# Kernel tuning notes

Measured on AMD Instinct MI355X. Metric: run time of the kernel, lower is better.

## Reference

```python
import jax, jax.numpy as jnp
import numpy as np

B, A, N, P, D, H = 2, 9, 1024, 4, 256, 8
DH = D // H
EPS = 1e-12


def _layernorm(x, gamma, beta):
    m = jnp.mean(x, axis=-1, keepdims=True)
    v = jnp.var(x, axis=-1, keepdims=True)
    return (x - m) / jnp.sqrt(v + EPS) * gamma + beta


def setup_inputs() -> dict:
    key = jax.random.key(0)
    ks = jax.random.split(key, 10)
    # adjacency stacks A relation matrices; scale 1/N keeps the P-step matmul chain O(1)
    adjacency = jax.random.uniform(ks[0], (B, A, N, N), jnp.float32) / N
    # diagonal, strictly positive degree matrix -> invertible
    diag = 1.0 + jax.random.uniform(ks[1], (B, N), jnp.float32)
    degree = jax.vmap(jnp.diag)(diag)
    x = jax.random.normal(ks[2], (B, N, D), jnp.float32)
    # per-head params stacked on leading H axis
    kernels = 0.1 * jax.random.normal(ks[3], (H, A, P), jnp.float32)  # RandomNormal(0, 0.1)
    lim = np.sqrt(6.0 / D).astype(np.float32)
    Wv = jax.random.uniform(ks[4], (H, D, DH), jnp.float32, -lim, lim)  # he_uniform
    Bv = jnp.zeros((H, N, DH), jnp.float32)
    W0 = jax.random.uniform(ks[5], (D, D), jnp.float32, -lim, lim)
    gamma2 = jnp.ones((D,), jnp.float32)
    beta2 = jnp.zeros((D,), jnp.float32)
    W1 = jax.random.normal(ks[6], (D, 2 * D), jnp.float32) * np.sqrt(2.0 / D).astype(np.float32)
    b1 = jnp.zeros((2 * D,), jnp.float32)
    gf = jnp.ones((2 * D,), jnp.float32)
    bf = jnp.zeros((2 * D,), jnp.float32)
    W2 = jax.random.normal(ks[7], (2 * D, D), jnp.float32) * np.sqrt(2.0 / (2 * D)).astype(np.float32)
    b2f = jnp.zeros((D,), jnp.float32)
    return {"adjacency": adjacency, "degree": degree, "x": x, "kernels": kernels,
            "Wv": Wv, "Bv": Bv, "W0": W0, "gamma2": gamma2, "beta2": beta2,
            "W1": W1, "b1": b1, "gf": gf, "bf": bf, "W2": W2, "b2f": b2f}


def reference(adjacency, degree, x, kernels, Wv, Bv, W0, gamma2, beta2, W1, b1, gf, bf, W2, b2f):
    # ---- AdjacencyAggregator (all H heads batched on leading axis) ----
    # softmax(relu(kernel)) over the input-channel (relation) axis
    soft = jax.nn.softmax(jax.nn.relu(kernels), axis=-2)  # [H, A, P]
    # 1x1 conv == per-position convex mix of the A relation matrices, one mix per path step
    # sequential chain: meta = M_0 @ M_1 @ ... @ M_{P-1}   (P is small and fixed)
    result = jnp.einsum('banm,ha->hbnm', adjacency, soft[:, :, 0])  # [H, B, N, N]
    for i in range(1, P):
        mi = jnp.einsum('banm,ha->hbnm', adjacency, soft[:, :, i])
        result = jnp.matmul(result, mi)
    inv_deg = jnp.linalg.inv(degree)                # [B, N, N], shared across heads
    normed = jnp.matmul(inv_deg[None], result)      # [H, B, N, N]
    # ---- MetaPathHead value projection + message passing ----
    V = jnp.einsum('bnd,hde->hbne', x, Wv) + Bv[:, None]   # [H, B, N, DH]
    heads = jnp.matmul(normed, V)                          # [H, B, N, DH]
    # concat along feature axis in head order
    attn = jnp.transpose(heads, (1, 2, 0, 3)).reshape(B, N, D)
    # ---- outer block: W0, residual, pre-norm FFN ----
    residual = attn @ W0 + x
    h = _layernorm(residual, gamma2, beta2)
    f = jax.nn.gelu(h @ W1 + b1, approximate=False)
    f = _layernorm(f, gf, bf)
    out = f @ W2 + b2f + residual
    return out
```

## Files before the change

### kernel.cpp

```cpp
#include <hip/hip_runtime.h>
#include <hip/hip_bf16.h>
#include <math.h>

#define B_ 2
#define A_ 9
#define N_ 1024
#define P_ 4
#define D_ 256
#define H_ 8
#define DH_ 32
#define ROWS_ (B_*N_)
#define KS_ 8
#define ADJ_ELEMS_ ((size_t)B_*A_*N_*N_)
#define SLABF4_ 131072

typedef __attribute__((ext_vector_type(8))) short bf16x8;
typedef __attribute__((ext_vector_type(4))) float f32x4;

__device__ __forceinline__ uint pack2_bf(float x, float y) {
    uint ux = __float_as_uint(x); ux += 0x7fffu + ((ux >> 16) & 1u);
    uint uy = __float_as_uint(y); uy += 0x7fffu + ((uy >> 16) & 1u);
    return (ux >> 16) | (uy & 0xffff0000u);
}
__device__ __forceinline__ float bflo(uint u){ return __uint_as_float(u << 16); }
__device__ __forceinline__ float bfhi(uint u){ return __uint_as_float(u & 0xffff0000u); }

__global__ void prep_kernel(const float* __restrict__ kernels, const float* __restrict__ degree,
                            float* __restrict__ soft, float* __restrict__ invd)
{
    int t = threadIdx.x;
    if (blockIdx.x == 0) {
        if (t < H_*P_) {
            int h = t >> 2, p = t & 3;
            float vals[A_];
            float m = 0.0f;
            #pragma unroll
            for (int a = 0; a < A_; a++) {
                float v = kernels[h*A_*P_ + a*P_ + p];
                v = v > 0.0f ? v : 0.0f;
                vals[a] = v;
                m = fmaxf(m, v);
            }
            float s = 0.0f;
            #pragma unroll
            for (int a = 0; a < A_; a++) { vals[a] = expf(vals[a] - m); s += vals[a]; }
            float inv = 1.0f / s;
            #pragma unroll
            for (int a = 0; a < A_; a++) soft[h*A_*P_ + a*P_ + p] = vals[a] * inv;
        }
    } else {
        int idx = (blockIdx.x - 1) * 256 + t;
        if (idx < ROWS_) {
            int b = idx >> 10, n = idx & (N_-1);
            invd[idx] = 1.0f / degree[(size_t)b*N_*N_ + (size_t)n*N_ + n];
        }
    }
}

__global__ void adj_pack_kernel(const float* __restrict__ in, ushort* __restrict__ out)
{
    int j = blockIdx.x * 256 + threadIdx.x;
    int kk8   = j & 3;
    int r     = (j >> 2) & 15;
    int t     = j >> 6;
    int a     = t % 9;
    int rest  = t / 9;
    int chunk = rest & 3;
    int ks    = (rest >> 2) & 7;
    int rowblk= (rest >> 5) & 63;
    int b     = rest >> 11;
    const float* src = &in[(((size_t)b*A_ + a)*N_ + (rowblk*16 + r))*N_ + ks*128 + chunk*32 + kk8*8];
    float4 v0 = *(const float4*)src;
    float4 v1 = *(const float4*)(src + 4);
    uint4 o;
    o.x = pack2_bf(v0.x, v0.y);
    o.y = pack2_bf(v0.z, v0.w);
    o.z = pack2_bf(v1.x, v1.y);
    o.w = pack2_bf(v1.z, v1.w);
    ((uint4*)out)[j] = o;
}

__global__ __launch_bounds__(256, 4)
void chain_mfma(const ushort* __restrict__ adjp, const float* __restrict__ soft,
                const ushort* __restrict__ Tin, float* __restrict__ Pp, int step)
{
    __shared__ __align__(16) ushort smem[8*640 + 16*648];
    __shared__ float soft_s[8][9];
    ushort* sm_ms = smem;
    ushort* sm_t  = smem + 8*640;

    int bid    = blockIdx.x;
    int ks     = bid & (KS_-1);
    int rowblk = (bid >> 3) & 63;
    int b      = bid >> 9;
    int n0     = rowblk * 16;
    int tid    = threadIdx.x;
    int lane   = tid & 63;
    int w      = tid >> 6;

    if (tid < 72) { int h = tid/9, a = tid%9; soft_s[h][a] = soft[h*A_*P_ + a*P_ + step]; }
    __syncthreads();

    int mr   = tid >> 4;
    int mk2  = (tid & 15) * 2;
    int mk2s = mk2 ^ ((mr & 3) << 3);
    const ushort* ablk = adjp + (size_t)((b*64 + rowblk)*8 + ks) * 18432;

    int sp  = tid >> 4;
    int sk0 = (tid & 15) * 2;
    const ushort* tbase = Tin + ((size_t)(b*16 + sp)*1024 + (size_t)ks*128) * 16;

    int g   = lane >> 4;
    int c15 = lane & 15;
    int gx  = (g ^ (c15 & 3)) * 8;

    f32x4 acc[4];
    #pragma unroll
    for (int j = 0; j < 4; j++) acc[j] = (f32x4){0.f, 0.f, 0.f, 0.f};

    for (int chunk = 0; chunk < 4; chunk++) {
        uint av[9];
        {
            const ushort* asl = ablk + chunk*4608 + mk2;
            #pragma unroll
            for (int a = 0; a < A_; a++) av[a] = *(const uint*)&asl[(a*16 + mr)*32];
        }
        const ushort* tsl = tbase + (size_t)(chunk*32 + sk0) * 16;
        uint4 q0 = *(const uint4*)(tsl + 0);
        uint4 q1 = *(const uint4*)(tsl + 8);
        uint4 q2 = *(const uint4*)(tsl + 16);
        uint4 q3 = *(const uint4*)(tsl + 24);

        if (chunk) __syncthreads();

        {
            float va0[9], va1[9];
            #pragma unroll
            for (int a = 0; a < A_; a++) { va0[a] = bflo(av[a]); va1[a] = bfhi(av[a]); }
            #pragma unroll
            for (int h = 0; h < H_; h++) {
                float s0 = soft_s[h][0]*va0[0];
                float s1 = soft_s[h][0]*va1[0];
                #pragma unroll
                for (int a = 1; a < A_; a++) { s0 += soft_s[h][a]*va0[a]; s1 += soft_s[h][a]*va1[a]; }
                *(uint*)&sm_ms[h*640 + mr*40 + mk2s] = pack2_bf(s0, s1);
            }
        }
        {
            uint l0[4] = {q0.x, q0.y, q0.z, q0.w};
            uint l1[4] = {q1.x, q1.y, q1.z, q1.w};
            uint h0[4] = {q2.x, q2.y, q2.z, q2.w};
            uint h1[4] = {q3.x, q3.y, q3.z, q3.w};
            #pragma unroll
            for (int ci = 0; ci < 8; ci++) {
                uint a0 = (l0[ci>>1] >> ((ci&1)*16)) & 0xffffu;
                uint b0 = (h0[ci>>1] >> ((ci&1)*16)) & 0xffffu;
                int k0s = sk0 ^ ((ci & 3) << 3);
                *(uint*)&sm_t[sp*648 + ci*40 + k0s] = a0 | (b0 << 16);
            }
            #pragma unroll
            for (int ci = 0; ci < 8; ci++) {
                int c = ci + 8;
                uint a0 = (l1[ci>>1] >> ((ci&1)*16)) & 0xffffu;
                uint b0 = (h1[ci>>1] >> ((ci&1)*16)) & 0xffffu;
                int k0s = sk0 ^ ((c & 3) << 3);
                *(uint*)&sm_t[sp*648 + c*40 + k0s] = a0 | (b0 << 16);
            }
        }
        __syncthreads();

        {
            const ushort* mb = sm_ms + c15*40 + gx;
            const ushort* tb = sm_t  + c15*40 + gx;
            #pragma unroll
            for (int j = 0; j < 4; j++) {
                int cg = w + 4*j;
                int h  = cg >> 1;
                bf16x8 af  = *(const bf16x8*)&mb[h*640];
                bf16x8 bfr = *(const bf16x8*)&tb[cg*648];
                acc[j] = __builtin_amdgcn_mfma_f32_16x16x32_bf16(af, bfr, acc[j], 0, 0, 0);
            }
        }
    }

    __syncthreads();
    float* Ep = (float*)smem;
    #pragma unroll
    for (int j = 0; j < 4; j++) {
        int cg = w + 4*j;
        #pragma unroll
        for (int i = 0; i < 4; i++)
            Ep[cg*256 + (g*4 + i)*16 + c15] = acc[j][i];
    }
    __syncthreads();
    {
        int p = tid >> 4, r = tid & 15;
        float* dst = Pp + (((size_t)(ks*B_ + b)*16 + p)*N_ + (n0 + r)) * 16;
        const float* src = &Ep[p*256 + r*16];
        *(float4*)&dst[0]  = *(const float4*)&src[0];
        *(float4*)&dst[4]  = *(const float4*)&src[4];
        *(float4*)&dst[8]  = *(const float4*)&src[8];
        *(float4*)&dst[12] = *(const float4*)&src[12];
    }
}

template<int FINAL>
__global__ void chain_reduce(const float* __restrict__ Pp, ushort* __restrict__ outp,
                             const float* __restrict__ invd)
{
    int pidx = blockIdx.x * 256 + threadIdx.x;
    float4 s = make_float4(0.f, 0.f, 0.f, 0.f);
    #pragma unroll
    for (int ks = 0; ks < KS_; ks++) {
        float4 v = ((const float4*)Pp)[(size_t)ks*SLABF4_ + pidx];
        s.x += v.x; s.y += v.y; s.z += v.z; s.w += v.w;
    }
    if constexpr (FINAL) {
        int lin = pidx * 4;
        int n  = (lin >> 4) & (N_-1);
        int b  = lin >> 18;
        float sc = invd[b*N_ + n];
        s.x *= sc; s.y *= sc; s.z *= sc; s.w *= sc;
    }
    uint2 wv;
    wv.x = pack2_bf(s.x, s.y);
    wv.y = pack2_bf(s.z, s.w);
    ((uint2*)outp)[pidx] = wv;
}

#define BK 16
__global__ void gemm_v(const float* __restrict__ A, const float* __restrict__ Bm,
                       const float* __restrict__ bias, ushort* __restrict__ C)
{
    __shared__ __align__(16) float As[BK][68];
    __shared__ __align__(16) float Bs[BK][68];
    int m0 = blockIdx.x * 64;
    int n0 = blockIdx.y * 64;
    int tid = threadIdx.x;
    int tx = tid & 15, ty = tid >> 4;

    float acc[4][4];
    #pragma unroll
    for (int i = 0; i < 4; i++)
        #pragma unroll
        for (int j = 0; j < 4; j++) acc[i][j] = 0.0f;

    for (int k0 = 0; k0 < D_; k0 += BK) {
        {
            int m = tid >> 2;
            int k = (tid & 3) * 4;
            float4 v = *(const float4*)&A[(size_t)(m0+m)*D_ + k0 + k];
            As[k+0][m] = v.x; As[k+1][m] = v.y; As[k+2][m] = v.z; As[k+3][m] = v.w;
        }
        {
            int k = tid >> 4;
            int n = (tid & 15) * 4;
            int c = n0 + n; int h = c >> 5; int ee = c & 31;
            float4 v = *(const float4*)&Bm[(size_t)h*D_*DH_ + (size_t)(k0+k)*DH_ + ee];
            *(float4*)&Bs[k][n] = v;
        }
        __syncthreads();
        #pragma unroll
        for (int k = 0; k < BK; k++) {
            float4 a4 = *(const float4*)&As[k][ty*4];
            float4 b4 = *(const float4*)&Bs[k][tx*4];
            acc[0][0] += a4.x*b4.x; acc[0][1] += a4.x*b4.y; acc[0][2] += a4.x*b4.z; acc[0][3] += a4.x*b4.w;
            acc[1][0] += a4.y*b4.x; acc[1][1] += a4.y*b4.y; acc[1][2] += a4.y*b4.z; acc[1][3] += a4.y*b4.w;
            acc[2][0] += a4.z*b4.x; acc[2][1] += a4.z*b4.y; acc[2][2] += a4.z*b4.z; acc[2][3] += a4.z*b4.w;
            acc[3][0] += a4.w*b4.x; acc[3][1] += a4.w*b4.y; acc[3][2] += a4.w*b4.z; acc[3][3] += a4.w*b4.w;
        }
        __syncthreads();
    }

    #pragma unroll
    for (int i = 0; i < 4; i++) {
        int row  = m0 + ty*4 + i;
        int nloc = n0 + tx*4;
        float o[4];
        #pragma unroll
        for (int j = 0; j < 4; j++) {
            int c = nloc + j;
            int h = c >> 5, ee = c & 31, n = row & (N_-1);
            o[j] = acc[i][j] + bias[(size_t)h*N_*DH_ + (size_t)n*DH_ + ee];
        }
        int bb = row >> 10, n = row & (N_-1);
        int cg = nloc >> 4, cc = nloc & 15;
        uint2 wv;
        wv.x = pack2_bf(o[0], o[1]);
        wv.y = pack2_bf(o[2], o[3]);
        *(uint2*)&C[(((size_t)bb*16 + cg)*N_ + n)*16 + cc] = wv;
    }
}


__global__ __launch_bounds__(256, 2)
void gemm_r(const ushort* __restrict__ attnp, const float* __restrict__ W0,
            const float* __restrict__ x, const float* __restrict__ gamma,
            const float* __restrict__ beta, float* __restrict__ resid,
            ushort* __restrict__ hbuf)
{
    __shared__ __align__(16) ushort As[16*40];
    __shared__ __align__(16) ushort Bs[256*40];
    __shared__ float lnb[16*257];
    __shared__ float2 stat[16];

    int m0 = blockIdx.x * 16;
    int b16 = (m0 >> 10) * 16;
    int nb  = m0 & (N_-1);
    int tid = threadIdx.x;
    int lane = tid & 63;
    int w = tid >> 6;
    int g = lane >> 4, c15 = lane & 15;
    int gx = (g ^ (c15 & 3)) * 8;

    int am = tid >> 4, ak2 = (tid & 15) * 2;
    int apos = am*40 + ((((ak2>>3) ^ (am&3))) << 3) + (ak2 & 7);
    int bn8 = (tid & 31) * 8;
    int bkq = (tid >> 5) * 4;
    int bpos0 = (((bkq>>3)) << 3) + (bkq & 7);

    f32x4 acc[4];
    #pragma unroll
    for (int j = 0; j < 4; j++) acc[j] = (f32x4){0.f,0.f,0.f,0.f};

    for (int ks = 0; ks < 8; ks++) {
        int k0 = ks * 32;
        int k = k0 + ak2;
        uint av = *(const uint*)&attnp[(((size_t)(b16 + (k>>4)))*N_ + nb + am)*16 + (k & 15)];
        float4 lo[4], hi[4];
        #pragma unroll
        for (int i = 0; i < 4; i++) {
            lo[i] = *(const float4*)&W0[(size_t)(k0+bkq+i)*D_ + bn8];
            hi[i] = *(const float4*)&W0[(size_t)(k0+bkq+i)*D_ + bn8 + 4];
        }
        if (ks) __syncthreads();
        *(uint*)&As[apos] = av;
        #pragma unroll
        for (int jn = 0; jn < 8; jn++) {
            int n = bn8 + jn;
            float v0 = (jn<4)? ((const float*)&lo[0])[jn] : ((const float*)&hi[0])[jn-4];
            float v1 = (jn<4)? ((const float*)&lo[1])[jn] : ((const float*)&hi[1])[jn-4];
            float v2 = (jn<4)? ((const float*)&lo[2])[jn] : ((const float*)&hi[2])[jn-4];
            float v3 = (jn<4)? ((const float*)&lo[3])[jn] : ((const float*)&hi[3])[jn-4];
            uint2 wv; wv.x = pack2_bf(v0, v1); wv.y = pack2_bf(v2, v3);
            *(uint2*)&Bs[n*40 + (bpos0 ^ ((n&3)<<3))] = wv;
        }
        __syncthreads();
        const ushort* ab = As + c15*40 + gx;
        #pragma unroll
        for (int nt = 0; nt < 4; nt++) {
            int n = w*64 + nt*16 + c15;
            bf16x8 af  = *(const bf16x8*)ab;
            bf16x8 bfr = *(const bf16x8*)&Bs[n*40 + gx];
            acc[nt] = __builtin_amdgcn_mfma_f32_16x16x32_bf16(af, bfr, acc[nt], 0, 0, 0);
        }
    }
    __syncthreads();

    #pragma unroll
    for (int nt = 0; nt < 4; nt++) {
        int c = w*64 + nt*16 + c15;
        #pragma unroll
        for (int i = 0; i < 4; i++) {
            int r = g*4 + i;
            lnb[r*257 + c] = acc[nt][i] + x[(size_t)(m0+r)*D_ + c];
        }
    }
    __syncthreads();

    {
        int rr = tid >> 4, sl = tid & 15;
        float sum = 0.f, sq = 0.f;
        #pragma unroll
        for (int j = 0; j < 16; j++) {
            float v = lnb[rr*257 + sl + 16*j];
            sum += v; sq += v*v;
        }
        #pragma unroll
        for (int m = 1; m < 16; m <<= 1) { sum += __shfl_xor(sum, m); sq += __shfl_xor(sq, m); }
        if (sl == 0) {
            float mean = sum * (1.0f/D_);
            float var  = fmaxf(sq * (1.0f/D_) - mean*mean, 0.f);
            stat[rr] = make_float2(mean, rsqrtf(var + 1e-12f));
        }
    }
    __syncthreads();

    {
        int rr = tid & 15, s2 = tid >> 4;
        float2 ms = stat[rr];
        int c0 = s2 * 16;
        uint hw[8];
        #pragma unroll
        for (int q = 0; q < 4; q++) {
            int c = c0 + q*4;
            float4 v = *(const float4*)&lnb[rr*257 + c];
            *(float4*)&resid[(size_t)(m0+rr)*D_ + c] = v;
            float4 gm = *(const float4*)&gamma[c];
            float4 bt = *(const float4*)&beta[c];
            float h0 = (v.x - ms.x)*ms.y*gm.x + bt.x;
            float h1 = (v.y - ms.x)*ms.y*gm.y + bt.y;
            float h2 = (v.z - ms.x)*ms.y*gm.z + bt.z;
            float h3 = (v.w - ms.x)*ms.y*gm.w + bt.w;
            hw[2*q]   = pack2_bf(h0, h1);
            hw[2*q+1] = pack2_bf(h2, h3);
        }
        ushort* hp = &hbuf[(size_t)(m0+rr)*D_ + c0];
        *(uint4*)&hp[0] = make_uint4(hw[0], hw[1], hw[2], hw[3]);
        *(uint4*)&hp[8] = make_uint4(hw[4], hw[5], hw[6], hw[7]);
    }
}

__global__ __launch_bounds__(256, 2)
void gemm_f1(const ushort* __restrict__ hbuf, const float* __restrict__ W1,
             const float* __restrict__ b1, const float* __restrict__ gf,
             const float* __restrict__ bfv, ushort* __restrict__ fout)
{
    __shared__ __align__(16) ushort As[16*40];
    __shared__ __align__(16) ushort Bs[512*40];
    __shared__ float lnb[16*513];
    __shared__ float2 stat[16];

    int m0 = blockIdx.x * 16;
    int tid = threadIdx.x;
    int lane = tid & 63;
    int w = tid >> 6;
    int g = lane >> 4, c15 = lane & 15;
    int gx = (g ^ (c15 & 3)) * 8;

    int am = tid >> 4, ak2 = (tid & 15) * 2;
    int apos = am*40 + ((((ak2>>3) ^ (am&3))) << 3) + (ak2 & 7);
    int bn8 = (tid & 63) * 8;
    int bk8 = (tid >> 6) * 8;

    f32x4 acc[8];
    #pragma unroll
    for (int j = 0; j < 8; j++) acc[j] = (f32x4){0.f,0.f,0.f,0.f};

    for (int ks = 0; ks < 8; ks++) {
        int k0 = ks * 32;
        uint av = *(const uint*)&hbuf[(size_t)(m0+am)*D_ + k0 + ak2];
        float4 q[16];
        #pragma unroll
        for (int i = 0; i < 8; i++) {
            q[2*i]   = *(const float4*)&W1[(size_t)(k0+bk8+i)*(2*D_) + bn8];
            q[2*i+1] = *(const float4*)&W1[(size_t)(k0+bk8+i)*(2*D_) + bn8 + 4];
        }
        if (ks) __syncthreads();
        *(uint*)&As[apos] = av;
        #pragma unroll
        for (int jn = 0; jn < 8; jn++) {
            int n = bn8 + jn;
            float e0 = (jn<4)? ((const float*)&q[0])[jn]  : ((const float*)&q[1])[jn-4];
            float e1 = (jn<4)? ((const float*)&q[2])[jn]  : ((const float*)&q[3])[jn-4];
            float e2 = (jn<4)? ((const float*)&q[4])[jn]  : ((const float*)&q[5])[jn-4];
            float e3 = (jn<4)? ((const float*)&q[6])[jn]  : ((const float*)&q[7])[jn-4];
            float e4 = (jn<4)? ((const float*)&q[8])[jn]  : ((const float*)&q[9])[jn-4];
            float e5 = (jn<4)? ((const float*)&q[10])[jn] : ((const float*)&q[11])[jn-4];
            float e6 = (jn<4)? ((const float*)&q[12])[jn] : ((const float*)&q[13])[jn-4];
            float e7 = (jn<4)? ((const float*)&q[14])[jn] : ((const float*)&q[15])[jn-4];
            uint4 wv;
            wv.x = pack2_bf(e0, e1); wv.y = pack2_bf(e2, e3);
            wv.z = pack2_bf(e4, e5); wv.w = pack2_bf(e6, e7);
            *(uint4*)&Bs[n*40 + ((((bk8>>3) ^ (n&3))) << 3)] = wv;
        }
        __syncthreads();
        const ushort* ab = As + c15*40 + gx;
        #pragma unroll
        for (int nt = 0; nt < 8; nt++) {
            int n = w*128 + nt*16 + c15;
            bf16x8 af  = *(const bf16x8*)ab;
            bf16x8 bfr = *(const bf16x8*)&Bs[n*40 + gx];
            acc[nt] = __builtin_amdgcn_mfma_f32_16x16x32_bf16(af, bfr, acc[nt], 0, 0, 0);
        }
    }
    __syncthreads();

    #pragma unroll
    for (int nt = 0; nt < 8; nt++) {
        int c = w*128 + nt*16 + c15;
        float bias = b1[c];
        #pragma unroll
        for (int i = 0; i < 4; i++) {
            int r = g*4 + i;
            float v = acc[nt][i] + bias;
            v = 0.5f * v * (1.0f + erff(v * 0.70710678118654752f));
            lnb[r*513 + c] = v;
        }
    }
    __syncthreads();

    {
        int rr = tid >> 4, sl = tid & 15;
        float sum = 0.f, sq = 0.f;
        #pragma unroll
        for (int j = 0; j < 32; j++) {
            float v = lnb[rr*513 + sl + 16*j];
            sum += v; sq += v*v;
        }
        #pragma unroll
        for (int m = 1; m < 16; m <<= 1) { sum += __shfl_xor(sum, m); sq += __shfl_xor(sq, m); }
        if (sl == 0) {
            float mean = sum * (1.0f/(2*D_));
            float var  = fmaxf(sq * (1.0f/(2*D_)) - mean*mean, 0.f);
            stat[rr] = make_float2(mean, rsqrtf(var + 1e-12f));
        }
    }
    __syncthreads();

    {
        int rr = tid & 15, s2 = tid >> 4;
        float2 ms = stat[rr];
        int c0 = s2 * 32;
        #pragma unroll
        for (int q = 0; q < 8; q++) {
            int c = c0 + q*4;
            float4 v = *(const float4*)&lnb[rr*513 + c];
            float4 gm = *(const float4*)&gf[c];
            float4 bt = *(const float4*)&bfv[c];
            float h0 = (v.x - ms.x)*ms.y*gm.x + bt.x;
            float h1 = (v.y - ms.x)*ms.y*gm.y + bt.y;
            float h2 = (v.z - ms.x)*ms.y*gm.z + bt.z;
            float h3 = (v.w - ms.x)*ms.y*gm.w + bt.w;
            *(uint2*)&fout[(size_t)(m0+rr)*(2*D_) + c] = make_uint2(pack2_bf(h0,h1), pack2_bf(h2,h3));
        }
    }
}

__global__ __launch_bounds__(256, 2)
void gemm_f2(const ushort* __restrict__ fbuf, const float* __restrict__ W2,
             const float* __restrict__ b2f, const float* __restrict__ resid,
             float* __restrict__ outp)
{
    __shared__ __align__(16) ushort As[16*40];
    __shared__ __align__(16) ushort Bs[256*40];
    __shared__ float lnb[16*257];

    int m0 = blockIdx.x * 16;
    int tid = threadIdx.x;
    int lane = tid & 63;
    int w = tid >> 6;
    int g = lane >> 4, c15 = lane & 15;
    int gx = (g ^ (c15 & 3)) * 8;

    int am = tid >> 4, ak2 = (tid & 15) * 2;
    int apos = am*40 + ((((ak2>>3) ^ (am&3))) << 3) + (ak2 & 7);
    int bn8 = (tid & 31) * 8;
    int bkq = (tid >> 5) * 4;
    int bpos0 = (((bkq>>3)) << 3) + (bkq & 7);

    f32x4 acc[4];
    #pragma unroll
    for (int j = 0; j < 4; j++) acc[j] = (f32x4){0.f,0.f,0.f,0.f};

    for (int ks = 0; ks < 16; ks++) {
        int k0 = ks * 32;
        uint av = *(const uint*)&fbuf[(size_t)(m0+am)*(2*D_) + k0 + ak2];
        float4 lo[4], hi[4];
        #pragma unroll
        for (int i = 0; i < 4; i++) {
            lo[i] = *(const float4*)&W2[(size_t)(k0+bkq+i)*D_ + bn8];
            hi[i] = *(const float4*)&W2[(size_t)(k0+bkq+i)*D_ + bn8 + 4];
        }
        if (ks) __syncthreads();
        *(uint*)&As[apos] = av;
        #pragma unroll
        for (int jn = 0; jn < 8; jn++) {
            int n = bn8 + jn;
            float v0 = (jn<4)? ((const float*)&lo[0])[jn] : ((const float*)&hi[0])[jn-4];
            float v1 = (jn<4)? ((const float*)&lo[1])[jn] : ((const float*)&hi[1])[jn-4];
            float v2 = (jn<4)? ((const float*)&lo[2])[jn] : ((const float*)&hi[2])[jn-4];
            float v3 = (jn<4)? ((const float*)&lo[3])[jn] : ((const float*)&hi[3])[jn-4];
            uint2 wv; wv.x = pack2_bf(v0, v1); wv.y = pack2_bf(v2, v3);
            *(uint2*)&Bs[n*40 + (bpos0 ^ ((n&3)<<3))] = wv;
        }
        __syncthreads();
        const ushort* ab = As + c15*40 + gx;
        #pragma unroll
        for (int nt = 0; nt < 4; nt++) {
            int n = w*64 + nt*16 + c15;
            bf16x8 af  = *(const bf16x8*)ab;
            bf16x8 bfr = *(const bf16x8*)&Bs[n*40 + gx];
            acc[nt] = __builtin_amdgcn_mfma_f32_16x16x32_bf16(af, bfr, acc[nt], 0, 0, 0);
        }
    }
    __syncthreads();

    #pragma unroll
    for (int nt = 0; nt < 4; nt++) {
        int c = w*64 + nt*16 + c15;
        #pragma unroll
        for (int i = 0; i < 4; i++)
            lnb[(g*4+i)*257 + c] = acc[nt][i];
    }
    __syncthreads();

    {
        int rr = tid & 15, s2 = tid >> 4;
        int c0 = s2 * 16;
        #pragma unroll
        for (int q = 0; q < 4; q++) {
            int c = c0 + q*4;
            float4 v  = *(const float4*)&lnb[rr*257 + c];
            float4 bb = *(const float4*)&b2f[c];
            float4 rs = *(const float4*)&resid[(size_t)(m0+rr)*D_ + c];
            float4 o = make_float4(v.x+bb.x+rs.x, v.y+bb.y+rs.y, v.z+bb.z+rs.z, v.w+bb.w+rs.w);
            *(float4*)&outp[(size_t)(m0+rr)*D_ + c] = o;
        }
    }
}

extern "C" void kernel_launch(void* const* d_in, const int* in_sizes, int n_in,
                              void* d_out, int out_size, void* d_ws, size_t ws_size,
                              hipStream_t stream)
{
    const float* adj    = (const float*)d_in[0];
    const float* degree = (const float*)d_in[1];
    const float* x      = (const float*)d_in[2];
    const float* kern   = (const float*)d_in[3];
    const float* Wv     = (const float*)d_in[4];
    const float* Bv     = (const float*)d_in[5];
    const float* W0     = (const float*)d_in[6];
    const float* gamma2 = (const float*)d_in[7];
    const float* beta2  = (const float*)d_in[8];
    const float* W1     = (const float*)d_in[9];
    const float* b1     = (const float*)d_in[10];
    const float* gf     = (const float*)d_in[11];
    const float* bf_    = (const float*)d_in[12];
    const float* W2     = (const float*)d_in[13];
    const float* b2f    = (const float*)d_in[14];
    float* out = (float*)d_out;
    float* ws  = (float*)d_ws;

    size_t off = 0;
    float* soft  = ws + off; off += 512;
    float* invd  = ws + off; off += 2048;
    float* T0    = ws + off; off += (size_t)ROWS_*D_;
    float* T1    = ws + off; off += (size_t)ROWS_*D_;
    float* resid = ws + off; off += (size_t)ROWS_*D_;
    float* hbuf  = ws + off; off += (size_t)ROWS_*D_;
    float* fbuf  = ws + off; off += (size_t)ROWS_*2*D_;
    float* fbuf2 = ws + off; off += (size_t)ROWS_*2*D_;
    float* Pp    = ws + off; off += (size_t)KS_*ROWS_*D_;
    ushort* adjp = (ushort*)(ws + off);
    (void)fbuf2;

    ushort* T0b = (ushort*)T0;
    ushort* T1b = (ushort*)T1;
    ushort* hb  = (ushort*)hbuf;
    ushort* fb  = (ushort*)fbuf;

    prep_kernel<<<9, 256, 0, stream>>>(kern, degree, soft, invd);
    adj_pack_kernel<<<(int)(ADJ_ELEMS_/8/256), 256, 0, stream>>>(adj, adjp);
    gemm_v<<<dim3(ROWS_/64, D_/64), 256, 0, stream>>>(x, Wv, Bv, T0b);

    int chain_grid  = B_*64*KS_;
    int reduce_grid = SLABF4_/256;
    chain_mfma<<<chain_grid, 256, 0, stream>>>(adjp, soft, T0b, Pp, 3);
    chain_reduce<0><<<reduce_grid, 256, 0, stream>>>(Pp, T1b, invd);
    chain_mfma<<<chain_grid, 256, 0, stream>>>(adjp, soft, T1b, Pp, 2);
    chain_reduce<0><<<reduce_grid, 256, 0, stream>>>(Pp, T0b, invd);
    chain_mfma<<<chain_grid, 256, 0, stream>>>(adjp, soft, T0b, Pp, 1);
    chain_reduce<0><<<reduce_grid, 256, 0, stream>>>(Pp, T1b, invd);
    chain_mfma<<<chain_grid, 256, 0, stream>>>(adjp, soft, T1b, Pp, 0);
    chain_reduce<1><<<reduce_grid, 256, 0, stream>>>(Pp, T0b, invd);

    gemm_r <<<ROWS_/16, 256, 0, stream>>>(T0b, W0, x, gamma2, beta2, resid, hb);
    gemm_f1<<<ROWS_/16, 256, 0, stream>>>(hb, W1, b1, gf, bf_, fb);
    gemm_f2<<<ROWS_/16, 256, 0, stream>>>(fb, W2, b2f, resid, out);
}
```

Before: 200.5 us.

## Fuse adjacency bf16 packing into first chain step and final reduce into W0 GEMM

Removes the separate adjacency pack kernel: the first chain_mfma step reads fp32 adjacency directly, uses it, and writes the packed bf16 copy that later steps read. The last split-K reduce and the inverse-degree scaling move into gemm_r, which sums the eight partial slabs while loading its A tile. The three tail GEMMs switch from 16 to 8 rows per block with higher occupancy bounds, so they launch twice as many blocks, but half the threads sit idle in the A load and epilogue phases.

```diff
diff --git a/kernel.cpp b/kernel.cpp
--- a/kernel.cpp
+++ b/kernel.cpp
@@ -12,7 +12,8 @@
 #define ROWS_ (B_*N_)
 #define KS_ 8
 #define ADJ_ELEMS_ ((size_t)B_*A_*N_*N_)
-#define SLABF4_ 131072
+#define SLABF_ 524288
+#define SLABF4_ (SLABF_/4)
 
 typedef __attribute__((ext_vector_type(8))) short bf16x8;
 typedef __attribute__((ext_vector_type(4))) float f32x4;
@@ -57,31 +58,10 @@
     }
 }
 
-__global__ void adj_pack_kernel(const float* __restrict__ in, ushort* __restrict__ out)
-{
-    int j = blockIdx.x * 256 + threadIdx.x;
-    int kk8   = j & 3;
-    int r     = (j >> 2) & 15;
-    int t     = j >> 6;
-    int a     = t % 9;
-    int rest  = t / 9;
-    int chunk = rest & 3;
-    int ks    = (rest >> 2) & 7;
-    int rowblk= (rest >> 5) & 63;
-    int b     = rest >> 11;
-    const float* src = &in[(((size_t)b*A_ + a)*N_ + (rowblk*16 + r))*N_ + ks*128 + chunk*32 + kk8*8];
-    float4 v0 = *(const float4*)src;
-    float4 v1 = *(const float4*)(src + 4);
-    uint4 o;
-    o.x = pack2_bf(v0.x, v0.y);
-    o.y = pack2_bf(v0.z, v0.w);
-    o.z = pack2_bf(v1.x, v1.y);
-    o.w = pack2_bf(v1.z, v1.w);
-    ((uint4*)out)[j] = o;
-}
-
+template<int PACK>
 __global__ __launch_bounds__(256, 4)
-void chain_mfma(const ushort* __restrict__ adjp, const float* __restrict__ soft,
+void chain_mfma(const float* __restrict__ adjf, ushort* __restrict__ adjp,
+                const float* __restrict__ soft,
                 const ushort* __restrict__ Tin, float* __restrict__ Pp, int step)
 {
     __shared__ __align__(16) ushort smem[8*640 + 16*648];
@@ -104,7 +84,7 @@
     int mr   = tid >> 4;
     int mk2  = (tid & 15) * 2;
     int mk2s = mk2 ^ ((mr & 3) << 3);
-    const ushort* ablk = adjp + (size_t)((b*64 + rowblk)*8 + ks) * 18432;
+    ushort* ablk = adjp + (size_t)((b*64 + rowblk)*8 + ks) * 18432;
 
     int sp  = tid >> 4;
     int sk0 = (tid & 15) * 2;
@@ -119,11 +99,20 @@
     for (int j = 0; j < 4; j++) acc[j] = (f32x4){0.f, 0.f, 0.f, 0.f};
 
     for (int chunk = 0; chunk < 4; chunk++) {
-        uint av[9];
-        {
-            const ushort* asl = ablk + chunk*4608 + mk2;
-            #pragma unroll
-            for (int a = 0; a < A_; a++) av[a] = *(const uint*)&asl[(a*16 + mr)*32];
+        float lo[9], hi[9];
+        if constexpr (PACK) {
+            #pragma unroll
+            for (int a = 0; a < A_; a++) {
+                float2 v = *(const float2*)&adjf[(((size_t)b*A_ + a)*N_ + (n0+mr))*N_
+                                                 + ks*128 + chunk*32 + mk2];
+                lo[a] = v.x; hi[a] = v.y;
+            }
+        } else {
+            #pragma unroll
+            for (int a = 0; a < A_; a++) {
+                uint av = *(const uint*)&ablk[chunk*4608 + (a*16 + mr)*32 + mk2];
+                lo[a] = bflo(av); hi[a] = bfhi(av);
+            }
         }
         const ushort* tsl = tbase + (size_t)(chunk*32 + sk0) * 16;
         uint4 q0 = *(const uint4*)(tsl + 0);
@@ -131,20 +120,21 @@
         uint4 q2 = *(const uint4*)(tsl + 16);
         uint4 q3 = *(const uint4*)(tsl + 24);
 
+        if constexpr (PACK) {
+            #pragma unroll
+            for (int a = 0; a < A_; a++)
+                *(uint*)&ablk[chunk*4608 + (a*16 + mr)*32 + mk2] = pack2_bf(lo[a], hi[a]);
+        }
+
         if (chunk) __syncthreads();
 
-        {
-            float va0[9], va1[9];
-            #pragma unroll
-            for (int a = 0; a < A_; a++) { va0[a] = bflo(av[a]); va1[a] = bfhi(av[a]); }
-            #pragma unroll
-            for (int h = 0; h < H_; h++) {
-                float s0 = soft_s[h][0]*va0[0];
-                float s1 = soft_s[h][0]*va1[0];
-                #pragma unroll
-                for (int a = 1; a < A_; a++) { s0 += soft_s[h][a]*va0[a]; s1 += soft_s[h][a]*va1[a]; }
-                *(uint*)&sm_ms[h*640 + mr*40 + mk2s] = pack2_bf(s0, s1);
-            }
+        #pragma unroll
+        for (int h = 0; h < H_; h++) {
+            float s0 = soft_s[h][0]*lo[0];
+            float s1 = soft_s[h][0]*hi[0];
+            #pragma unroll
+            for (int a = 1; a < A_; a++) { s0 += soft_s[h][a]*lo[a]; s1 += soft_s[h][a]*hi[a]; }
+            *(uint*)&sm_ms[h*640 + mr*40 + mk2s] = pack2_bf(s0, s1);
         }
         {
             uint l0[4] = {q0.x, q0.y, q0.z, q0.w};
@@ -204,9 +194,7 @@
     }
 }
 
-template<int FINAL>
-__global__ void chain_reduce(const float* __restrict__ Pp, ushort* __restrict__ outp,
-                             const float* __restrict__ invd)
+__global__ void chain_reduce(const float* __restrict__ Pp, ushort* __restrict__ outp)
 {
     int pidx = blockIdx.x * 256 + threadIdx.x;
     float4 s = make_float4(0.f, 0.f, 0.f, 0.f);
@@ -214,13 +202,6 @@
     for (int ks = 0; ks < KS_; ks++) {
         float4 v = ((const float4*)Pp)[(size_t)ks*SLABF4_ + pidx];
         s.x += v.x; s.y += v.y; s.z += v.z; s.w += v.w;
-    }
-    if constexpr (FINAL) {
-        int lin = pidx * 4;
-        int n  = (lin >> 4) & (N_-1);
-        int b  = lin >> 18;
-        float sc = invd[b*N_ + n];
-        s.x *= sc; s.y *= sc; s.z *= sc; s.w *= sc;
     }
     uint2 wv;
     wv.x = pack2_bf(s.x, s.y);
@@ -293,48 +274,61 @@
 }
 
 
-__global__ __launch_bounds__(256, 2)
-void gemm_r(const ushort* __restrict__ attnp, const float* __restrict__ W0,
-            const float* __restrict__ x, const float* __restrict__ gamma,
-            const float* __restrict__ beta, float* __restrict__ resid,
-            ushort* __restrict__ hbuf)
+__global__ __launch_bounds__(256, 4)
+void gemm_r(const float* __restrict__ Pp, const float* __restrict__ invd,
+            const float* __restrict__ W0, const float* __restrict__ x,
+            const float* __restrict__ gamma, const float* __restrict__ beta,
+            float* __restrict__ resid, ushort* __restrict__ hbuf)
 {
     __shared__ __align__(16) ushort As[16*40];
     __shared__ __align__(16) ushort Bs[256*40];
-    __shared__ float lnb[16*257];
-    __shared__ float2 stat[16];
-
-    int m0 = blockIdx.x * 16;
-    int b16 = (m0 >> 10) * 16;
-    int nb  = m0 & (N_-1);
+    __shared__ float lnb[8*257];
+    __shared__ float2 stat[8];
+
+    int m0 = blockIdx.x * 8;
+    int b  = m0 >> 10;
+    int nb = m0 & (N_-1);
     int tid = threadIdx.x;
     int lane = tid & 63;
     int w = tid >> 6;
     int g = lane >> 4, c15 = lane & 15;
     int gx = (g ^ (c15 & 3)) * 8;
 
-    int am = tid >> 4, ak2 = (tid & 15) * 2;
+    int am  = tid >> 4;
+    int ak2 = (tid & 15) * 2;
     int apos = am*40 + ((((ak2>>3) ^ (am&3))) << 3) + (ak2 & 7);
+    float idv = (tid < 128) ? invd[b*N_ + nb + am] : 0.f;
+
     int bn8 = (tid & 31) * 8;
     int bkq = (tid >> 5) * 4;
-    int bpos0 = (((bkq>>3)) << 3) + (bkq & 7);
+    int bposR = ((bkq >> 3) << 3) + (bkq & 7);
 
     f32x4 acc[4];
     #pragma unroll
     for (int j = 0; j < 4; j++) acc[j] = (f32x4){0.f,0.f,0.f,0.f};
 
-    for (int ks = 0; ks < 8; ks++) {
-        int k0 = ks * 32;
-        int k = k0 + ak2;
-        uint av = *(const uint*)&attnp[(((size_t)(b16 + (k>>4)))*N_ + nb + am)*16 + (k & 15)];
+    for (int ksi = 0; ksi < 8; ksi++) {
+        int k0 = ksi * 32;
+        uint av = 0;
+        if (tid < 128) {
+            int k = k0 + ak2;
+            size_t base = (((size_t)(b*16 + (k>>4)))*N_ + nb + am)*16 + (k & 15);
+            float s0 = 0.f, s1 = 0.f;
+            #pragma unroll
+            for (int sl = 0; sl < 8; sl++) {
+                float2 v = *(const float2*)&Pp[(size_t)sl*SLABF_ + base];
+                s0 += v.x; s1 += v.y;
+            }
+            av = pack2_bf(s0*idv, s1*idv);
+        }
         float4 lo[4], hi[4];
         #pragma unroll
         for (int i = 0; i < 4; i++) {
             lo[i] = *(const float4*)&W0[(size_t)(k0+bkq+i)*D_ + bn8];
             hi[i] = *(const float4*)&W0[(size_t)(k0+bkq+i)*D_ + bn8 + 4];
         }
-        if (ks) __syncthreads();
-        *(uint*)&As[apos] = av;
+        if (ksi) __syncthreads();
+        if (tid < 128) *(uint*)&As[apos] = av;
         #pragma unroll
         for (int jn = 0; jn < 8; jn++) {
             int n = bn8 + jn;
@@ -343,7 +337,7 @@
             float v2 = (jn<4)? ((const float*)&lo[2])[jn] : ((const float*)&hi[2])[jn-4];
             float v3 = (jn<4)? ((const float*)&lo[3])[jn] : ((const float*)&hi[3])[jn-4];
             uint2 wv; wv.x = pack2_bf(v0, v1); wv.y = pack2_bf(v2, v3);
-            *(uint2*)&Bs[n*40 + (bpos0 ^ ((n&3)<<3))] = wv;
+            *(uint2*)&Bs[n*40 + (bposR ^ ((n&3)<<3))] = wv;
         }
         __syncthreads();
         const ushort* ab = As + c15*40 + gx;
@@ -357,18 +351,19 @@
     }
     __syncthreads();
 
-    #pragma unroll
-    for (int nt = 0; nt < 4; nt++) {
-        int c = w*64 + nt*16 + c15;
-        #pragma unroll
-        for (int i = 0; i < 4; i++) {
-            int r = g*4 + i;
-            lnb[r*257 + c] = acc[nt][i] + x[(size_t)(m0+r)*D_ + c];
-        }
-    }
-    __syncthreads();
-
-    {
+    if (g < 2) {
+        #pragma unroll
+        for (int nt = 0; nt < 4; nt++) {
+            int c = w*64 + nt*16 + c15;
+            #pragma unroll
+            for (int i = 0; i < 4; i++) {
+                int r = g*4 + i;
+                lnb[r*257 + c] = acc[nt][i] + x[(size_t)(m0+r)*D_ + c];
+            }
+        }
+    }
+    __syncthreads();
+    if (tid < 128) {
         int rr = tid >> 4, sl = tid & 15;
         float sum = 0.f, sq = 0.f;
         #pragma unroll
@@ -385,9 +380,8 @@
         }
     }
     __syncthreads();
-
-    {
-        int rr = tid & 15, s2 = tid >> 4;
+    if (tid < 128) {
+        int rr = tid & 7, s2 = tid >> 3;
         float2 ms = stat[rr];
         int c0 = s2 * 16;
         uint hw[8];
@@ -418,36 +412,38 @@
 {
     __shared__ __align__(16) ushort As[16*40];
     __shared__ __align__(16) ushort Bs[512*40];
-    __shared__ float lnb[16*513];
-    __shared__ float2 stat[16];
-
-    int m0 = blockIdx.x * 16;
+    __shared__ float lnb[8*513];
+    __shared__ float2 stat[8];
+
+    int m0 = blockIdx.x * 8;
     int tid = threadIdx.x;
     int lane = tid & 63;
     int w = tid >> 6;
     int g = lane >> 4, c15 = lane & 15;
     int gx = (g ^ (c15 & 3)) * 8;
 
-    int am = tid >> 4, ak2 = (tid & 15) * 2;
+    int am  = tid >> 4;
+    int ak2 = (tid & 15) * 2;
     int apos = am*40 + ((((ak2>>3) ^ (am&3))) << 3) + (ak2 & 7);
     int bn8 = (tid & 63) * 8;
     int bk8 = (tid >> 6) * 8;
 
-    f32x4 acc[8];
-    #pragma unroll
-    for (int j = 0; j < 8; j++) acc[j] = (f32x4){0.f,0.f,0.f,0.f};
-
-    for (int ks = 0; ks < 8; ks++) {
-        int k0 = ks * 32;
-        uint av = *(const uint*)&hbuf[(size_t)(m0+am)*D_ + k0 + ak2];
+    f32x4 acc1[8];
+    #pragma unroll
+    for (int j = 0; j < 8; j++) acc1[j] = (f32x4){0.f,0.f,0.f,0.f};
+
+    for (int ksi = 0; ksi < 8; ksi++) {
+        int k0 = ksi * 32;
+        uint av = 0;
+        if (tid < 128) av = *(const uint*)&hbuf[(size_t)(m0+am)*D_ + k0 + ak2];
         float4 q[16];
         #pragma unroll
         for (int i = 0; i < 8; i++) {
             q[2*i]   = *(const float4*)&W1[(size_t)(k0+bk8+i)*(2*D_) + bn8];
             q[2*i+1] = *(const float4*)&W1[(size_t)(k0+bk8+i)*(2*D_) + bn8 + 4];
         }
-        if (ks) __syncthreads();
-        *(uint*)&As[apos] = av;
+        if (ksi) __syncthreads();
+        if (tid < 128) *(uint*)&As[apos] = av;
         #pragma unroll
         for (int jn = 0; jn < 8; jn++) {
             int n = bn8 + jn;
@@ -471,26 +467,27 @@
             int n = w*128 + nt*16 + c15;
             bf16x8 af  = *(const bf16x8*)ab;
             bf16x8 bfr = *(const bf16x8*)&Bs[n*40 + gx];
-            acc[nt] = __builtin_amdgcn_mfma_f32_16x16x32_bf16(af, bfr, acc[nt], 0, 0, 0);
-        }
-    }
-    __syncthreads();
-
-    #pragma unroll
-    for (int nt = 0; nt < 8; nt++) {
-        int c = w*128 + nt*16 + c15;
-        float bias = b1[c];
-        #pragma unroll
-        for (int i = 0; i < 4; i++) {
-            int r = g*4 + i;
-            float v = acc[nt][i] + bias;
-            v = 0.5f * v * (1.0f + erff(v * 0.70710678118654752f));
-            lnb[r*513 + c] = v;
-        }
-    }
-    __syncthreads();
-
-    {
+            acc1[nt] = __builtin_amdgcn_mfma_f32_16x16x32_bf16(af, bfr, acc1[nt], 0, 0, 0);
+        }
+    }
+    __syncthreads();
+
+    if (g < 2) {
+        #pragma unroll
+        for (int nt = 0; nt < 8; nt++) {
+            int c = w*128 + nt*16 + c15;
+            float bias = b1[c];
+            #pragma unroll
+            for (int i = 0; i < 4; i++) {
+                int r = g*4 + i;
+                float v = acc1[nt][i] + bias;
+                v = 0.5f * v * (1.0f + erff(v * 0.70710678118654752f));
+                lnb[r*513 + c] = v;
+            }
+        }
+    }
+    __syncthreads();
+    if (tid < 128) {
         int rr = tid >> 4, sl = tid & 15;
         float sum = 0.f, sq = 0.f;
         #pragma unroll
@@ -507,9 +504,8 @@
         }
     }
     __syncthreads();
-
-    {
-        int rr = tid & 15, s2 = tid >> 4;
+    if (tid < 128) {
+        int rr = tid & 7, s2 = tid >> 3;
         float2 ms = stat[rr];
         int c0 = s2 * 32;
         #pragma unroll
@@ -527,43 +523,45 @@
     }
 }
 
-__global__ __launch_bounds__(256, 2)
+__global__ __launch_bounds__(256, 4)
 void gemm_f2(const ushort* __restrict__ fbuf, const float* __restrict__ W2,
              const float* __restrict__ b2f, const float* __restrict__ resid,
              float* __restrict__ outp)
 {
     __shared__ __align__(16) ushort As[16*40];
     __shared__ __align__(16) ushort Bs[256*40];
-    __shared__ float lnb[16*257];
-
-    int m0 = blockIdx.x * 16;
+    __shared__ float esc[8*257];
+
+    int m0 = blockIdx.x * 8;
     int tid = threadIdx.x;
     int lane = tid & 63;
     int w = tid >> 6;
     int g = lane >> 4, c15 = lane & 15;
     int gx = (g ^ (c15 & 3)) * 8;
 
-    int am = tid >> 4, ak2 = (tid & 15) * 2;
+    int am  = tid >> 4;
+    int ak2 = (tid & 15) * 2;
     int apos = am*40 + ((((ak2>>3) ^ (am&3))) << 3) + (ak2 & 7);
     int bn8 = (tid & 31) * 8;
     int bkq = (tid >> 5) * 4;
-    int bpos0 = (((bkq>>3)) << 3) + (bkq & 7);
+    int bposR = ((bkq >> 3) << 3) + (bkq & 7);
 
     f32x4 acc[4];
     #pragma unroll
     for (int j = 0; j < 4; j++) acc[j] = (f32x4){0.f,0.f,0.f,0.f};
 
-    for (int ks = 0; ks < 16; ks++) {
-        int k0 = ks * 32;
-        uint av = *(const uint*)&fbuf[(size_t)(m0+am)*(2*D_) + k0 + ak2];
+    for (int ksi = 0; ksi < 16; ksi++) {
+        int k0 = ksi * 32;
+        uint av = 0;
+        if (tid < 128) av = *(const uint*)&fbuf[(size_t)(m0+am)*(2*D_) + k0 + ak2];
         float4 lo[4], hi[4];
         #pragma unroll
         for (int i = 0; i < 4; i++) {
             lo[i] = *(const float4*)&W2[(size_t)(k0+bkq+i)*D_ + bn8];
             hi[i] = *(const float4*)&W2[(size_t)(k0+bkq+i)*D_ + bn8 + 4];
         }
-        if (ks) __syncthreads();
-        *(uint*)&As[apos] = av;
+        if (ksi) __syncthreads();
+        if (tid < 128) *(uint*)&As[apos] = av;
         #pragma unroll
         for (int jn = 0; jn < 8; jn++) {
             int n = bn8 + jn;
@@ -572,7 +570,7 @@
             float v2 = (jn<4)? ((const float*)&lo[2])[jn] : ((const float*)&hi[2])[jn-4];
             float v3 = (jn<4)? ((const float*)&lo[3])[jn] : ((const float*)&hi[3])[jn-4];
             uint2 wv; wv.x = pack2_bf(v0, v1); wv.y = pack2_bf(v2, v3);
-            *(uint2*)&Bs[n*40 + (bpos0 ^ ((n&3)<<3))] = wv;
+            *(uint2*)&Bs[n*40 + (bposR ^ ((n&3)<<3))] = wv;
         }
         __syncthreads();
         const ushort* ab = As + c15*40 + gx;
@@ -586,22 +584,23 @@
     }
     __syncthreads();
 
-    #pragma unroll
-    for (int nt = 0; nt < 4; nt++) {
-        int c = w*64 + nt*16 + c15;
-        #pragma unroll
-        for (int i = 0; i < 4; i++)
-            lnb[(g*4+i)*257 + c] = acc[nt][i];
-    }
-    __syncthreads();
-
-    {
-        int rr = tid & 15, s2 = tid >> 4;
+    if (g < 2) {
+        #pragma unroll
+        for (int nt = 0; nt < 4; nt++) {
+            int c = w*64 + nt*16 + c15;
+            #pragma unroll
+            for (int i = 0; i < 4; i++)
+                esc[(g*4+i)*257 + c] = acc[nt][i];
+        }
+    }
+    __syncthreads();
+    if (tid < 128) {
+        int rr = tid & 7, s2 = tid >> 3;
         int c0 = s2 * 16;
         #pragma unroll
         for (int q = 0; q < 4; q++) {
             int c = c0 + q*4;
-            float4 v  = *(const float4*)&lnb[rr*257 + c];
+            float4 v  = *(const float4*)&esc[rr*257 + c];
             float4 bb = *(const float4*)&b2f[c];
             float4 rs = *(const float4*)&resid[(size_t)(m0+rr)*D_ + c];
             float4 o = make_float4(v.x+bb.x+rs.x, v.y+bb.y+rs.y, v.z+bb.z+rs.z, v.w+bb.w+rs.w);
@@ -638,34 +637,30 @@
     float* T0    = ws + off; off += (size_t)ROWS_*D_;
     float* T1    = ws + off; off += (size_t)ROWS_*D_;
     float* resid = ws + off; off += (size_t)ROWS_*D_;
-    float* hbuf  = ws + off; off += (size_t)ROWS_*D_;
-    float* fbuf  = ws + off; off += (size_t)ROWS_*2*D_;
-    float* fbuf2 = ws + off; off += (size_t)ROWS_*2*D_;
+    float* hbufF = ws + off; off += (size_t)ROWS_*D_/2;
+    float* foutF = ws + off; off += (size_t)ROWS_*D_;
     float* Pp    = ws + off; off += (size_t)KS_*ROWS_*D_;
     ushort* adjp = (ushort*)(ws + off);
-    (void)fbuf2;
 
     ushort* T0b = (ushort*)T0;
     ushort* T1b = (ushort*)T1;
-    ushort* hb  = (ushort*)hbuf;
-    ushort* fb  = (ushort*)fbuf;
+    ushort* hb  = (ushort*)hbufF;
+    ushort* fb  = (ushort*)foutF;
 
     prep_kernel<<<9, 256, 0, stream>>>(kern, degree, soft, invd);
-    adj_pack_kernel<<<(int)(ADJ_ELEMS_/8/256), 256, 0, stream>>>(adj, adjp);
     gemm_v<<<dim3(ROWS_/64, D_/64), 256, 0, stream>>>(x, Wv, Bv, T0b);
 
     int chain_grid  = B_*64*KS_;
     int reduce_grid = SLABF4_/256;
-    chain_mfma<<<chain_grid, 256, 0, stream>>>(adjp, soft, T0b, Pp, 3);
-    chain_reduce<0><<<reduce_grid, 256, 0, stream>>>(Pp, T1b, invd);
-    chain_mfma<<<chain_grid, 256, 0, stream>>>(adjp, soft, T1b, Pp, 2);
-    chain_reduce<0><<<reduce_grid, 256, 0, stream>>>(Pp, T0b, invd);
-    chain_mfma<<<chain_grid, 256, 0, stream>>>(adjp, soft, T0b, Pp, 1);
-    chain_reduce<0><<<reduce_grid, 256, 0, stream>>>(Pp, T1b, invd);
-    chain_mfma<<<chain_grid, 256, 0, stream>>>(adjp, soft, T1b, Pp, 0);
-    chain_reduce<1><<<reduce_grid, 256, 0, stream>>>(Pp, T0b, invd);
-
-    gemm_r <<<ROWS_/16, 256, 0, stream>>>(T0b, W0, x, gamma2, beta2, resid, hb);
-    gemm_f1<<<ROWS_/16, 256, 0, stream>>>(hb, W1, b1, gf, bf_, fb);
-    gemm_f2<<<ROWS_/16, 256, 0, stream>>>(fb, W2, b2f, resid, out);
-}
+    chain_mfma<1><<<chain_grid, 256, 0, stream>>>(adj, adjp, soft, T0b, Pp, 3);
+    chain_reduce<<<reduce_grid, 256, 0, stream>>>(Pp, T1b);
+    chain_mfma<0><<<chain_grid, 256, 0, stream>>>(adj, adjp, soft, T1b, Pp, 2);
+    chain_reduce<<<reduce_grid, 256, 0, stream>>>(Pp, T0b);
+    chain_mfma<0><<<chain_grid, 256, 0, stream>>>(adj, adjp, soft, T0b, Pp, 1);
+    chain_reduce<<<reduce_grid, 256, 0, stream>>>(Pp, T1b);
+    chain_mfma<0><<<chain_grid, 256, 0, stream>>>(adj, adjp, soft, T1b, Pp, 0);
+
+    gemm_r <<<ROWS_/8, 256, 0, stream>>>(Pp, invd, W0, x, gamma2, beta2, resid, hb);
+    gemm_f1<<<ROWS_/8, 256, 0, stream>>>(hb, W1, b1, gf, bf_, fb);
+    gemm_f2<<<ROWS_/8, 256, 0, stream>>>(fb, W2, b2f, resid, out);
+}
```

New measurement: 182.6 us. -8.9%, faster.
